# Performance work log

Hardware: AMD Instinct MI355X
Metric: run time of the kernel (lower is better)

## Reference

```python
import jax, jax.numpy as jnp
import numpy as np

EPS = 1e-5  # torch LayerNorm default
N_BLOCKS = 8
N_NODES = 4096
BATCH = 4096


def setup_inputs() -> dict:
    key = jax.random.key(0)
    ks = jax.random.split(key, 4)
    scale = 1.0 / np.sqrt(N_NODES)  # keep activations sane through 8 GEMMs
    x = jax.random.normal(ks[0], (BATCH, N_NODES), dtype=jnp.float32)
    W = jax.random.normal(ks[1], (N_BLOCKS, N_NODES, N_NODES), dtype=jnp.float32) * scale
    b = jax.random.normal(ks[2], (N_BLOCKS, N_NODES), dtype=jnp.float32) * 0.01
    slope = jax.random.uniform(ks[3], (N_BLOCKS, N_NODES), dtype=jnp.float32)
    ln_g = jnp.ones((N_BLOCKS, N_NODES), dtype=jnp.float32)
    ln_b = jnp.zeros((N_BLOCKS, N_NODES), dtype=jnp.float32)
    return {"x": x, "ln_g": ln_g, "ln_b": ln_b, "W": W, "b": b, "slope": slope}


def _block(x, g, bt, Wi, bi, si):
    # LayerNorm over last dim (biased variance, eps inside sqrt) -> Linear -> per-feature LeakyReLU
    mu = jnp.mean(x, axis=-1, keepdims=True)
    var = jnp.mean(jnp.square(x - mu), axis=-1, keepdims=True)
    ln = (x - mu) * jax.lax.rsqrt(var + EPS) * g + bt
    y = jnp.einsum('bn,mn->bm', ln, Wi) + bi  # torch Linear: x @ W.T + b
    return jnp.where(y < 0, y * si, y)


def reference(x, ln_g, ln_b, W, b, slope):
    for i in range(N_BLOCKS):
        x = _block(x, ln_g[i], ln_b[i], W[i], b[i], slope[i])
    return x
```

## Files before the change

### kernel.cpp

```cpp
#include <hip/hip_runtime.h>
#include <hip/hip_bf16.h>

#define NNODES 4096
#define NBATCH 4096
#define NBLK 8
#define LN_EPS 1e-5f

typedef __attribute__((ext_vector_type(8))) short short8;
typedef __attribute__((ext_vector_type(4))) float f32x4;
typedef __attribute__((ext_vector_type(4))) unsigned short u16x4;
typedef unsigned short u16;

__device__ __forceinline__ u16 bf16_rn(float f) {
  unsigned int u = __builtin_bit_cast(unsigned int, f);
  u += 0x7fffu + ((u >> 16) & 1u);
  return (u16)(u >> 16);
}

__device__ __forceinline__ float bf16_to_f(u16 h) {
  unsigned int u = ((unsigned int)h) << 16;
  return __builtin_bit_cast(float, u);
}

__device__ __forceinline__ void load_lds16(const void* g, void* l) {
  __builtin_amdgcn_global_load_lds((const __attribute__((address_space(1))) void*)g,
                                   (__attribute__((address_space(3))) void*)l,
                                   16, 0, 0);
}

__device__ __forceinline__ void stage_sub(const u16* g, u16* l) {
  load_lds16(g, l);
  load_lds16(g + (size_t)128 * NNODES, l + 4096);
}

__global__ __launch_bounds__(256) void convw_kernel(const float* __restrict__ W,
                                                    u16* __restrict__ Wb) {
  int idx = blockIdx.x * 256 + threadIdx.x;
  float4 v = ((const float4*)W)[idx];
  u16x4 o;
  o[0] = bf16_rn(v.x); o[1] = bf16_rn(v.y); o[2] = bf16_rn(v.z); o[3] = bf16_rn(v.w);
  ((u16x4*)Wb)[idx] = o;
}

__global__ __launch_bounds__(256) void ln_f32_kernel(const float* __restrict__ x,
                                                     const float* __restrict__ g,
                                                     const float* __restrict__ bt,
                                                     u16* __restrict__ out) {
  int row = blockIdx.x;
  int t = threadIdx.x;
  const float4* xr = (const float4*)(x + (size_t)row * NNODES);
  float4 v[4];
  float s = 0.f, ss = 0.f;
#pragma unroll
  for (int q = 0; q < 4; ++q) {
    v[q] = xr[q * 256 + t];
    s  += v[q].x + v[q].y + v[q].z + v[q].w;
    ss += v[q].x * v[q].x + v[q].y * v[q].y + v[q].z * v[q].z + v[q].w * v[q].w;
  }
#pragma unroll
  for (int off = 32; off >= 1; off >>= 1) {
    s  += __shfl_xor(s, off, 64);
    ss += __shfl_xor(ss, off, 64);
  }
  __shared__ float sh[8];
  int wid = t >> 6, lane = t & 63;
  if (lane == 0) { sh[wid] = s; sh[wid + 4] = ss; }
  __syncthreads();
  s  = sh[0] + sh[1] + sh[2] + sh[3];
  ss = sh[4] + sh[5] + sh[6] + sh[7];
  float mu  = s * (1.f / NNODES);
  float var = ss * (1.f / NNODES) - mu * mu;
  float rs  = rsqrtf(var + LN_EPS);
  u16x4* o = (u16x4*)(out + (size_t)row * NNODES);
  const float4* gv = (const float4*)g;
  const float4* bv = (const float4*)bt;
#pragma unroll
  for (int q = 0; q < 4; ++q) {
    int i = q * 256 + t;
    float4 gg = gv[i], bb = bv[i];
    u16x4 ov;
    ov[0] = bf16_rn((v[q].x - mu) * rs * gg.x + bb.x);
    ov[1] = bf16_rn((v[q].y - mu) * rs * gg.y + bb.y);
    ov[2] = bf16_rn((v[q].z - mu) * rs * gg.z + bb.z);
    ov[3] = bf16_rn((v[q].w - mu) * rs * gg.w + bb.w);
    o[i] = ov;
  }
}

__global__ __launch_bounds__(256) void ln_bf16_kernel(const u16* __restrict__ x,
                                                      const float* __restrict__ g,
                                                      const float* __restrict__ bt,
                                                      u16* __restrict__ out) {
  int row = blockIdx.x;
  int t = threadIdx.x;
  const u16* xr = x + (size_t)row * NNODES;
  float f[2][8];
  float s = 0.f, ss = 0.f;
#pragma unroll
  for (int q = 0; q < 2; ++q) {
    short8 v = *(const short8*)(xr + q * 2048 + t * 8);
#pragma unroll
    for (int j = 0; j < 8; ++j) {
      float fv = bf16_to_f((u16)v[j]);
      f[q][j] = fv;
      s += fv; ss += fv * fv;
    }
  }
#pragma unroll
  for (int off = 32; off >= 1; off >>= 1) {
    s  += __shfl_xor(s, off, 64);
    ss += __shfl_xor(ss, off, 64);
  }
  __shared__ float sh[8];
  int wid = t >> 6, lane = t & 63;
  if (lane == 0) { sh[wid] = s; sh[wid + 4] = ss; }
  __syncthreads();
  s  = sh[0] + sh[1] + sh[2] + sh[3];
  ss = sh[4] + sh[5] + sh[6] + sh[7];
  float mu  = s * (1.f / NNODES);
  float var = ss * (1.f / NNODES) - mu * mu;
  float rs  = rsqrtf(var + LN_EPS);
  const float4* gv = (const float4*)g;
  const float4* bv = (const float4*)bt;
#pragma unroll
  for (int q = 0; q < 2; ++q) {
    int base = q * 2048 + t * 8;
    float4 g0 = gv[base / 4], g1 = gv[base / 4 + 1];
    float4 b0 = bv[base / 4], b1 = bv[base / 4 + 1];
    short8 sv;
    sv[0] = (short)bf16_rn((f[q][0] - mu) * rs * g0.x + b0.x);
    sv[1] = (short)bf16_rn((f[q][1] - mu) * rs * g0.y + b0.y);
    sv[2] = (short)bf16_rn((f[q][2] - mu) * rs * g0.z + b0.z);
    sv[3] = (short)bf16_rn((f[q][3] - mu) * rs * g0.w + b0.w);
    sv[4] = (short)bf16_rn((f[q][4] - mu) * rs * g1.x + b1.x);
    sv[5] = (short)bf16_rn((f[q][5] - mu) * rs * g1.y + b1.y);
    sv[6] = (short)bf16_rn((f[q][6] - mu) * rs * g1.z + b1.z);
    sv[7] = (short)bf16_rn((f[q][7] - mu) * rs * g1.w + b1.w);
    *(short8*)(out + (size_t)row * NNODES + base) = sv;
  }
}

template <bool OUTF32>
__global__ __launch_bounds__(512, 2) void gemm256_kernel(const u16* __restrict__ A,
                                                         const u16* __restrict__ B,
                                                         const float* __restrict__ bias,
                                                         const float* __restrict__ slope,
                                                         void* __restrict__ Cv) {
  constexpr int Kdim = NNODES;
  constexpr int NSUB = Kdim / 32;
  __shared__ u16 Alds[4][8192];
  __shared__ u16 Blds[4][8192];

  const int tid  = threadIdx.x;
  const int lane = tid & 63;
  const int wid  = tid >> 6;
  const int wr   = wid >> 2;
  const int wc   = wid & 3;

  int bid = blockIdx.x;
  int swz = (bid & 7) * 32 + (bid >> 3);
  const int brow = (swz >> 4) * 256;
  const int bcol = (swz & 15) * 256;

  const int srow = tid >> 2;
  const int scsw = (tid & 3) ^ ((srow >> 1) & 3);
  const u16* Ag = A + (size_t)(brow + srow) * Kdim + scsw * 8;
  const u16* Bg = B + (size_t)(bcol + srow) * Kdim + scsw * 8;

  const int r16 = lane & 15, kq = lane >> 4;
  const int ck  = kq ^ ((r16 >> 1) & 3);
  const int aoff = (wr * 128 + r16) * 32 + ck * 8;
  const int boff = (wc * 64 + r16) * 32 + ck * 8;

  f32x4 acc[8][4] = {};

#pragma unroll
  for (int s = 0; s < 3; ++s) {
    stage_sub(Ag + s * 32, &Alds[s][0] + tid * 8);
    stage_sub(Bg + s * 32, &Blds[s][0] + tid * 8);
  }
  asm volatile("s_waitcnt vmcnt(8)" ::: "memory");
  __builtin_amdgcn_s_barrier();

  for (int s = 0; s < NSUB; ++s) {
    const int sl = s & 3;
    const u16* abase = &Alds[sl][0] + aoff;
    const u16* bbase = &Blds[sl][0] + boff;
    short8 afr[4], bfr[4];

#pragma unroll
    for (int n = 0; n < 4; ++n) bfr[n] = *(const short8*)(bbase + n * 512);
#pragma unroll
    for (int m = 0; m < 4; ++m) afr[m] = *(const short8*)(abase + m * 512);
    if (s + 3 < NSUB) stage_sub(Ag + (s + 3) * 32, &Alds[(s + 3) & 3][0] + tid * 8);
    asm volatile("s_waitcnt lgkmcnt(0)" ::: "memory");
    __builtin_amdgcn_sched_barrier(0);
    __builtin_amdgcn_s_setprio(1);
#pragma unroll
    for (int m = 0; m < 4; ++m)
#pragma unroll
      for (int n = 0; n < 4; ++n)
        acc[m][n] = __builtin_amdgcn_mfma_f32_16x16x32_bf16(afr[m], bfr[n], acc[m][n], 0, 0, 0);
    __builtin_amdgcn_s_setprio(0);

#pragma unroll
    for (int m = 0; m < 4; ++m) afr[m] = *(const short8*)(abase + (m + 4) * 512);
    if (s + 3 < NSUB) stage_sub(Bg + (s + 3) * 32, &Blds[(s + 3) & 3][0] + tid * 8);
    if (s <= NSUB - 4)      asm volatile("s_waitcnt vmcnt(8)" ::: "memory");
    else if (s == NSUB - 3) asm volatile("s_waitcnt vmcnt(4)" ::: "memory");
    else if (s == NSUB - 2) asm volatile("s_waitcnt vmcnt(0)" ::: "memory");
    asm volatile("s_waitcnt lgkmcnt(0)" ::: "memory");
    __builtin_amdgcn_sched_barrier(0);
    __builtin_amdgcn_s_setprio(1);
#pragma unroll
    for (int m = 0; m < 4; ++m)
#pragma unroll
      for (int n = 0; n < 4; ++n)
        acc[m + 4][n] = __builtin_amdgcn_mfma_f32_16x16x32_bf16(afr[m], bfr[n], acc[m + 4][n], 0, 0, 0);
    __builtin_amdgcn_s_setprio(0);
    __builtin_amdgcn_s_barrier();
  }

  const int crow0 = brow + wr * 128 + (lane >> 4) * 4;
  const int ccol0 = bcol + wc * 64 + r16;
#pragma unroll
  for (int n = 0; n < 4; ++n) {
    int col = ccol0 + n * 16;
    float bv = bias[col], sv = slope[col];
#pragma unroll
    for (int m = 0; m < 8; ++m) {
      int row0 = crow0 + m * 16;
#pragma unroll
      for (int r = 0; r < 4; ++r) {
        float vv = acc[m][n][r] + bv;
        vv = vv < 0.f ? vv * sv : vv;
        if constexpr (OUTF32) {
          ((float*)Cv)[(size_t)(row0 + r) * NNODES + col] = vv;
        } else {
          ((u16*)Cv)[(size_t)(row0 + r) * NNODES + col] = bf16_rn(vv);
        }
      }
    }
  }
}

extern "C" void kernel_launch(void* const* d_in, const int* in_sizes, int n_in,
                              void* d_out, int out_size, void* d_ws, size_t ws_size,
                              hipStream_t stream) {
  const float* x     = (const float*)d_in[0];
  const float* ln_g  = (const float*)d_in[1];
  const float* ln_b  = (const float*)d_in[2];
  const float* W     = (const float*)d_in[3];
  const float* b     = (const float*)d_in[4];
  const float* slope = (const float*)d_in[5];
  float* out = (float*)d_out;

  char* ws = (char*)d_ws;
  u16* Wbuf  = (u16*)ws;
  u16* lnbuf = (u16*)(ws + (size_t)32 * 1024 * 1024);
  u16* ybuf  = (u16*)(ws + (size_t)64 * 1024 * 1024);

  const size_t WN = (size_t)NNODES * NNODES;

  for (int i = 0; i < NBLK; ++i) {
    convw_kernel<<<dim3(WN / 4 / 256), dim3(256), 0, stream>>>(W + WN * i, Wbuf);
    if (i == 0)
      ln_f32_kernel<<<dim3(NBATCH), dim3(256), 0, stream>>>(x, ln_g, ln_b, lnbuf);
    else
      ln_bf16_kernel<<<dim3(NBATCH), dim3(256), 0, stream>>>(ybuf, ln_g + (size_t)i * NNODES,
                                                             ln_b + (size_t)i * NNODES, lnbuf);
    if (i == NBLK - 1)
      gemm256_kernel<true><<<dim3(256), dim3(512), 0, stream>>>(lnbuf, Wbuf,
                                                                b + (size_t)i * NNODES,
                                                                slope + (size_t)i * NNODES, (void*)out);
    else
      gemm256_kernel<false><<<dim3(256), dim3(512), 0, stream>>>(lnbuf, Wbuf,
                                                                 b + (size_t)i * NNODES,
                                                                 slope + (size_t)i * NNODES, (void*)ybuf);
  }
}
```

Baseline: 1.229 ms.

## Fuse weight conversion with LayerNorm and restructure GEMM LDS read schedule

Merges the per-block fp32→bf16 weight conversion and the LayerNorm into one launch, with block-index ranges choosing the role. This cuts the launch count and lets both memory-bound phases run at the same time. The GEMM main loop now issues all A fragment LDS reads and both global→LDS stages up front. It then waits on lgkmcnt(4) so the first MFMA half can start while the second A half is still loading. The trade-off is more live registers for the extra fragment array.

```diff
diff --git a/kernel.cpp b/kernel.cpp
--- a/kernel.cpp
+++ b/kernel.cpp
@@ -33,36 +33,53 @@
   load_lds16(g + (size_t)128 * NNODES, l + 4096);
 }
 
-__global__ __launch_bounds__(256) void convw_kernel(const float* __restrict__ W,
-                                                    u16* __restrict__ Wb) {
-  int idx = blockIdx.x * 256 + threadIdx.x;
-  float4 v = ((const float4*)W)[idx];
-  u16x4 o;
-  o[0] = bf16_rn(v.x); o[1] = bf16_rn(v.y); o[2] = bf16_rn(v.z); o[3] = bf16_rn(v.w);
-  ((u16x4*)Wb)[idx] = o;
-}
-
-__global__ __launch_bounds__(256) void ln_f32_kernel(const float* __restrict__ x,
-                                                     const float* __restrict__ g,
-                                                     const float* __restrict__ bt,
-                                                     u16* __restrict__ out) {
-  int row = blockIdx.x;
+template <bool LNF32>
+__global__ __launch_bounds__(256) void prep_kernel(const float* __restrict__ W,
+                                                   u16* __restrict__ Wb,
+                                                   const void* __restrict__ xin,
+                                                   const float* __restrict__ g,
+                                                   const float* __restrict__ bt,
+                                                   u16* __restrict__ lnout) {
+  __shared__ float sh[8];
   int t = threadIdx.x;
-  const float4* xr = (const float4*)(x + (size_t)row * NNODES);
-  float4 v[4];
+  if (blockIdx.x < 16384) {
+    int idx = blockIdx.x * 256 + t;
+    float4 v = ((const float4*)W)[idx];
+    u16x4 o;
+    o[0] = bf16_rn(v.x); o[1] = bf16_rn(v.y); o[2] = bf16_rn(v.z); o[3] = bf16_rn(v.w);
+    ((u16x4*)Wb)[idx] = o;
+    return;
+  }
+  int row = blockIdx.x - 16384;
+  float f[16];
   float s = 0.f, ss = 0.f;
-#pragma unroll
-  for (int q = 0; q < 4; ++q) {
-    v[q] = xr[q * 256 + t];
-    s  += v[q].x + v[q].y + v[q].z + v[q].w;
-    ss += v[q].x * v[q].x + v[q].y * v[q].y + v[q].z * v[q].z + v[q].w * v[q].w;
+  if constexpr (LNF32) {
+    const float4* xr = (const float4*)((const float*)xin + (size_t)row * NNODES);
+#pragma unroll
+    for (int q = 0; q < 4; ++q) {
+      float4 v = xr[q * 256 + t];
+      f[q * 4 + 0] = v.x; f[q * 4 + 1] = v.y; f[q * 4 + 2] = v.z; f[q * 4 + 3] = v.w;
+      s  += v.x + v.y + v.z + v.w;
+      ss += v.x * v.x + v.y * v.y + v.z * v.z + v.w * v.w;
+    }
+  } else {
+    const u16* xr = (const u16*)xin + (size_t)row * NNODES;
+#pragma unroll
+    for (int q = 0; q < 2; ++q) {
+      short8 v = *(const short8*)(xr + q * 2048 + t * 8);
+#pragma unroll
+      for (int j = 0; j < 8; ++j) {
+        float fv = bf16_to_f((u16)v[j]);
+        f[q * 8 + j] = fv;
+        s += fv; ss += fv * fv;
+      }
+    }
   }
 #pragma unroll
   for (int off = 32; off >= 1; off >>= 1) {
     s  += __shfl_xor(s, off, 64);
     ss += __shfl_xor(ss, off, 64);
   }
-  __shared__ float sh[8];
   int wid = t >> 6, lane = t & 63;
   if (lane == 0) { sh[wid] = s; sh[wid + 4] = ss; }
   __syncthreads();
@@ -71,72 +88,40 @@
   float mu  = s * (1.f / NNODES);
   float var = ss * (1.f / NNODES) - mu * mu;
   float rs  = rsqrtf(var + LN_EPS);
-  u16x4* o = (u16x4*)(out + (size_t)row * NNODES);
-  const float4* gv = (const float4*)g;
-  const float4* bv = (const float4*)bt;
-#pragma unroll
-  for (int q = 0; q < 4; ++q) {
-    int i = q * 256 + t;
-    float4 gg = gv[i], bb = bv[i];
-    u16x4 ov;
-    ov[0] = bf16_rn((v[q].x - mu) * rs * gg.x + bb.x);
-    ov[1] = bf16_rn((v[q].y - mu) * rs * gg.y + bb.y);
-    ov[2] = bf16_rn((v[q].z - mu) * rs * gg.z + bb.z);
-    ov[3] = bf16_rn((v[q].w - mu) * rs * gg.w + bb.w);
-    o[i] = ov;
-  }
-}
-
-__global__ __launch_bounds__(256) void ln_bf16_kernel(const u16* __restrict__ x,
-                                                      const float* __restrict__ g,
-                                                      const float* __restrict__ bt,
-                                                      u16* __restrict__ out) {
-  int row = blockIdx.x;
-  int t = threadIdx.x;
-  const u16* xr = x + (size_t)row * NNODES;
-  float f[2][8];
-  float s = 0.f, ss = 0.f;
-#pragma unroll
-  for (int q = 0; q < 2; ++q) {
-    short8 v = *(const short8*)(xr + q * 2048 + t * 8);
-#pragma unroll
-    for (int j = 0; j < 8; ++j) {
-      float fv = bf16_to_f((u16)v[j]);
-      f[q][j] = fv;
-      s += fv; ss += fv * fv;
-    }
-  }
-#pragma unroll
-  for (int off = 32; off >= 1; off >>= 1) {
-    s  += __shfl_xor(s, off, 64);
-    ss += __shfl_xor(ss, off, 64);
-  }
-  __shared__ float sh[8];
-  int wid = t >> 6, lane = t & 63;
-  if (lane == 0) { sh[wid] = s; sh[wid + 4] = ss; }
-  __syncthreads();
-  s  = sh[0] + sh[1] + sh[2] + sh[3];
-  ss = sh[4] + sh[5] + sh[6] + sh[7];
-  float mu  = s * (1.f / NNODES);
-  float var = ss * (1.f / NNODES) - mu * mu;
-  float rs  = rsqrtf(var + LN_EPS);
-  const float4* gv = (const float4*)g;
-  const float4* bv = (const float4*)bt;
-#pragma unroll
-  for (int q = 0; q < 2; ++q) {
-    int base = q * 2048 + t * 8;
-    float4 g0 = gv[base / 4], g1 = gv[base / 4 + 1];
-    float4 b0 = bv[base / 4], b1 = bv[base / 4 + 1];
-    short8 sv;
-    sv[0] = (short)bf16_rn((f[q][0] - mu) * rs * g0.x + b0.x);
-    sv[1] = (short)bf16_rn((f[q][1] - mu) * rs * g0.y + b0.y);
-    sv[2] = (short)bf16_rn((f[q][2] - mu) * rs * g0.z + b0.z);
-    sv[3] = (short)bf16_rn((f[q][3] - mu) * rs * g0.w + b0.w);
-    sv[4] = (short)bf16_rn((f[q][4] - mu) * rs * g1.x + b1.x);
-    sv[5] = (short)bf16_rn((f[q][5] - mu) * rs * g1.y + b1.y);
-    sv[6] = (short)bf16_rn((f[q][6] - mu) * rs * g1.z + b1.z);
-    sv[7] = (short)bf16_rn((f[q][7] - mu) * rs * g1.w + b1.w);
-    *(short8*)(out + (size_t)row * NNODES + base) = sv;
+  const float* gp = g;
+  const float* bp = bt;
+  if constexpr (LNF32) {
+    u16x4* o = (u16x4*)(lnout + (size_t)row * NNODES);
+    const float4* gv = (const float4*)gp;
+    const float4* bv = (const float4*)bp;
+#pragma unroll
+    for (int q = 0; q < 4; ++q) {
+      int i = q * 256 + t;
+      float4 gg = gv[i], bb = bv[i];
+      u16x4 ov;
+      ov[0] = bf16_rn((f[q * 4 + 0] - mu) * rs * gg.x + bb.x);
+      ov[1] = bf16_rn((f[q * 4 + 1] - mu) * rs * gg.y + bb.y);
+      ov[2] = bf16_rn((f[q * 4 + 2] - mu) * rs * gg.z + bb.z);
+      ov[3] = bf16_rn((f[q * 4 + 3] - mu) * rs * gg.w + bb.w);
+      o[i] = ov;
+    }
+  } else {
+#pragma unroll
+    for (int q = 0; q < 2; ++q) {
+      int base = q * 2048 + t * 8;
+      float4 g0 = ((const float4*)gp)[base / 4], g1 = ((const float4*)gp)[base / 4 + 1];
+      float4 b0 = ((const float4*)bp)[base / 4], b1 = ((const float4*)bp)[base / 4 + 1];
+      short8 sv;
+      sv[0] = (short)bf16_rn((f[q * 8 + 0] - mu) * rs * g0.x + b0.x);
+      sv[1] = (short)bf16_rn((f[q * 8 + 1] - mu) * rs * g0.y + b0.y);
+      sv[2] = (short)bf16_rn((f[q * 8 + 2] - mu) * rs * g0.z + b0.z);
+      sv[3] = (short)bf16_rn((f[q * 8 + 3] - mu) * rs * g0.w + b0.w);
+      sv[4] = (short)bf16_rn((f[q * 8 + 4] - mu) * rs * g1.x + b1.x);
+      sv[5] = (short)bf16_rn((f[q * 8 + 5] - mu) * rs * g1.y + b1.y);
+      sv[6] = (short)bf16_rn((f[q * 8 + 6] - mu) * rs * g1.z + b1.z);
+      sv[7] = (short)bf16_rn((f[q * 8 + 7] - mu) * rs * g1.w + b1.w);
+      *(short8*)(lnout + (size_t)row * NNODES + base) = sv;
+    }
   }
 }
 
@@ -186,13 +171,34 @@
     const int sl = s & 3;
     const u16* abase = &Alds[sl][0] + aoff;
     const u16* bbase = &Blds[sl][0] + boff;
-    short8 afr[4], bfr[4];
+    short8 a03[4], a47[4], bfr[4];
 
 #pragma unroll
     for (int n = 0; n < 4; ++n) bfr[n] = *(const short8*)(bbase + n * 512);
 #pragma unroll
-    for (int m = 0; m < 4; ++m) afr[m] = *(const short8*)(abase + m * 512);
-    if (s + 3 < NSUB) stage_sub(Ag + (s + 3) * 32, &Alds[(s + 3) & 3][0] + tid * 8);
+    for (int m = 0; m < 4; ++m) a03[m] = *(const short8*)(abase + m * 512);
+    __builtin_amdgcn_sched_barrier(0);
+#pragma unroll
+    for (int m = 0; m < 4; ++m) a47[m] = *(const short8*)(abase + (m + 4) * 512);
+
+    if (s + 3 < NSUB) {
+      stage_sub(Ag + (s + 3) * 32, &Alds[(s + 3) & 3][0] + tid * 8);
+      stage_sub(Bg + (s + 3) * 32, &Blds[(s + 3) & 3][0] + tid * 8);
+    }
+    if (s <= NSUB - 4)      asm volatile("s_waitcnt vmcnt(8)" ::: "memory");
+    else if (s == NSUB - 3) asm volatile("s_waitcnt vmcnt(4)" ::: "memory");
+    else if (s == NSUB - 2) asm volatile("s_waitcnt vmcnt(0)" ::: "memory");
+
+    asm volatile("s_waitcnt lgkmcnt(4)" ::: "memory");
+    __builtin_amdgcn_sched_barrier(0);
+    __builtin_amdgcn_s_setprio(1);
+#pragma unroll
+    for (int m = 0; m < 4; ++m)
+#pragma unroll
+      for (int n = 0; n < 4; ++n)
+        acc[m][n] = __builtin_amdgcn_mfma_f32_16x16x32_bf16(a03[m], bfr[n], acc[m][n], 0, 0, 0);
+    __builtin_amdgcn_s_setprio(0);
+
     asm volatile("s_waitcnt lgkmcnt(0)" ::: "memory");
     __builtin_amdgcn_sched_barrier(0);
     __builtin_amdgcn_s_setprio(1);
@@ -200,23 +206,7 @@
     for (int m = 0; m < 4; ++m)
 #pragma unroll
       for (int n = 0; n < 4; ++n)
-        acc[m][n] = __builtin_amdgcn_mfma_f32_16x16x32_bf16(afr[m], bfr[n], acc[m][n], 0, 0, 0);
-    __builtin_amdgcn_s_setprio(0);
-
-#pragma unroll
-    for (int m = 0; m < 4; ++m) afr[m] = *(const short8*)(abase + (m + 4) * 512);
-    if (s + 3 < NSUB) stage_sub(Bg + (s + 3) * 32, &Blds[(s + 3) & 3][0] + tid * 8);
-    if (s <= NSUB - 4)      asm volatile("s_waitcnt vmcnt(8)" ::: "memory");
-    else if (s == NSUB - 3) asm volatile("s_waitcnt vmcnt(4)" ::: "memory");
-    else if (s == NSUB - 2) asm volatile("s_waitcnt vmcnt(0)" ::: "memory");
-    asm volatile("s_waitcnt lgkmcnt(0)" ::: "memory");
-    __builtin_amdgcn_sched_barrier(0);
-    __builtin_amdgcn_s_setprio(1);
-#pragma unroll
-    for (int m = 0; m < 4; ++m)
-#pragma unroll
-      for (int n = 0; n < 4; ++n)
-        acc[m + 4][n] = __builtin_amdgcn_mfma_f32_16x16x32_bf16(afr[m], bfr[n], acc[m + 4][n], 0, 0, 0);
+        acc[m + 4][n] = __builtin_amdgcn_mfma_f32_16x16x32_bf16(a47[m], bfr[n], acc[m + 4][n], 0, 0, 0);
     __builtin_amdgcn_s_setprio(0);
     __builtin_amdgcn_s_barrier();
   }
@@ -261,14 +251,16 @@
   u16* ybuf  = (u16*)(ws + (size_t)64 * 1024 * 1024);
 
   const size_t WN = (size_t)NNODES * NNODES;
+  const dim3 pgrid(16384 + NBATCH);
 
   for (int i = 0; i < NBLK; ++i) {
-    convw_kernel<<<dim3(WN / 4 / 256), dim3(256), 0, stream>>>(W + WN * i, Wbuf);
     if (i == 0)
-      ln_f32_kernel<<<dim3(NBATCH), dim3(256), 0, stream>>>(x, ln_g, ln_b, lnbuf);
+      prep_kernel<true><<<pgrid, dim3(256), 0, stream>>>(W, Wbuf, (const void*)x,
+                                                         ln_g, ln_b, lnbuf);
     else
-      ln_bf16_kernel<<<dim3(NBATCH), dim3(256), 0, stream>>>(ybuf, ln_g + (size_t)i * NNODES,
-                                                             ln_b + (size_t)i * NNODES, lnbuf);
+      prep_kernel<false><<<pgrid, dim3(256), 0, stream>>>(W + WN * i, Wbuf, (const void*)ybuf,
+                                                          ln_g + (size_t)i * NNODES,
+                                                          ln_b + (size_t)i * NNODES, lnbuf);
     if (i == NBLK - 1)
       gemm256_kernel<true><<<dim3(256), dim3(512), 0, stream>>>(lnbuf, Wbuf,
                                                                 b + (size_t)i * NNODES,
```

After: 1.182 ms. 3.8% less time.

## Fuse fp32-to-bf16 weight conversion into GEMM B-tile loading

Applied to the files above, without the earlier changes.

Removes the separate weight conversion kernel per block. The GEMM now loads fp32 weights into registers, converts them to bf16 and writes them into swizzled LDS, while A tiles still go straight to LDS via global_load_lds. The main loop is rebuilt into K=64 double-buffered tiles with quarter-tile phases that interleave loads, LDS writes and MFMAs. This saves a full read and write pass over each 64MB weight matrix, but the GEMM now reads twice as many bytes for B and pays extra VALU and register cost for the conversion.

```diff
diff --git a/kernel.cpp b/kernel.cpp
--- a/kernel.cpp
+++ b/kernel.cpp
@@ -28,18 +28,17 @@
                                    16, 0, 0);
 }
 
-__device__ __forceinline__ void stage_sub(const u16* g, u16* l) {
-  load_lds16(g, l);
-  load_lds16(g + (size_t)128 * NNODES, l + 4096);
-}
-
-__global__ __launch_bounds__(256) void convw_kernel(const float* __restrict__ W,
-                                                    u16* __restrict__ Wb) {
-  int idx = blockIdx.x * 256 + threadIdx.x;
-  float4 v = ((const float4*)W)[idx];
-  u16x4 o;
-  o[0] = bf16_rn(v.x); o[1] = bf16_rn(v.y); o[2] = bf16_rn(v.z); o[3] = bf16_rn(v.w);
-  ((u16x4*)Wb)[idx] = o;
+__device__ __forceinline__ void gload4(f32x4& d, const float* p) {
+  asm volatile("global_load_dwordx4 %0, %1, off" : "=&v"(d) : "v"(p) : "memory");
+}
+
+__device__ __forceinline__ short8 cvt8(f32x4 a, f32x4 b) {
+  short8 r;
+  r[0] = (short)bf16_rn(a[0]); r[1] = (short)bf16_rn(a[1]);
+  r[2] = (short)bf16_rn(a[2]); r[3] = (short)bf16_rn(a[3]);
+  r[4] = (short)bf16_rn(b[0]); r[5] = (short)bf16_rn(b[1]);
+  r[6] = (short)bf16_rn(b[2]); r[7] = (short)bf16_rn(b[3]);
+  return r;
 }
 
 __global__ __launch_bounds__(256) void ln_f32_kernel(const float* __restrict__ x,
@@ -140,16 +139,77 @@
   }
 }
 
+
+#define VMC(N) asm volatile("s_waitcnt vmcnt(" #N ")" ::: "memory")
+#define NOP ((void)0)
+
+#define STAGE_A(T, H)                                                          \
+  { load_lds16(Asrc0 + (size_t)((H) * 128) * Kdim + (T) * 64,                  \
+               ldsA + ((T) & 1) * 16384 + (H) * 8192 + tid * 8);               \
+    load_lds16(Asrc0 + (size_t)((H) * 128 + 64) * Kdim + (T) * 64,             \
+               ldsA + ((T) & 1) * 16384 + (H) * 8192 + 4096 + tid * 8); }
+
+#define LOADB(R, T, H)                                                         \
+  { const float* p_ = Wp + (size_t)((H) * 128 + bwrow) * Kdim + (T) * 64 + bwc4 * 16; \
+    gload4(R[0], p_); gload4(R[1], p_ + 4);                                    \
+    gload4(R[2], p_ + 8); gload4(R[3], p_ + 12); }
+
+#define WRITEB(R, T, H)                                                        \
+  { u16* d_ = ldsB + ((T) & 1) * 16384 + (H) * 8192 + bwrow * 64;              \
+    *(short8*)(d_ + bwg0 * 8) = cvt8(R[0], R[1]);                              \
+    *(short8*)(d_ + bwg1 * 8) = cvt8(R[2], R[3]);                              \
+    asm volatile("s_waitcnt lgkmcnt(0)" ::: "memory"); }
+
+#define PH(KT, MH, NH, EXTRA, VM_STMT, WR_STMT)                                \
+  {                                                                            \
+    EXTRA;                                                                     \
+    VM_STMT;                                                                   \
+    __builtin_amdgcn_sched_barrier(0);                                         \
+    WR_STMT;                                                                   \
+    __builtin_amdgcn_sched_barrier(0);                                         \
+    const u16* Ab = ldsA + ((KT) & 1) * 16384 + aBase + (MH) * 4096;           \
+    const u16* Bb = ldsB + ((KT) & 1) * 16384 + bBase + (NH) * 2048;           \
+    if ((NH) == 0) {                                                           \
+      _Pragma("unroll") for (int mi = 0; mi < 4; ++mi) {                       \
+        afr[mi][0] = *(const short8*)(Ab + mi * 1024 + gk0);                   \
+        afr[mi][1] = *(const short8*)(Ab + mi * 1024 + gk1);                   \
+      }                                                                        \
+    }                                                                          \
+    if ((MH) == 0) {                                                           \
+      _Pragma("unroll") for (int ni = 0; ni < 2; ++ni) {                       \
+        bfr[NH][ni][0] = *(const short8*)(Bb + ni * 1024 + gk0);               \
+        bfr[NH][ni][1] = *(const short8*)(Bb + ni * 1024 + gk1);               \
+      }                                                                        \
+    }                                                                          \
+    if ((NH) == 0 && (MH) == 0)                                                \
+      asm volatile("s_waitcnt lgkmcnt(8)" ::: "memory");                       \
+    __builtin_amdgcn_s_barrier();                                              \
+    asm volatile("s_waitcnt lgkmcnt(0)" ::: "memory");                         \
+    __builtin_amdgcn_sched_barrier(0);                                         \
+    __builtin_amdgcn_s_setprio(1);                                             \
+    _Pragma("unroll") for (int mi = 0; mi < 4; ++mi)                           \
+      _Pragma("unroll") for (int ni = 0; ni < 2; ++ni) {                       \
+        acc[(MH) * 4 + mi][(NH) * 2 + ni] =                                    \
+          __builtin_amdgcn_mfma_f32_16x16x32_bf16(afr[mi][0], bfr[NH][ni][0],  \
+            acc[(MH) * 4 + mi][(NH) * 2 + ni], 0, 0, 0);                       \
+        acc[(MH) * 4 + mi][(NH) * 2 + ni] =                                    \
+          __builtin_amdgcn_mfma_f32_16x16x32_bf16(afr[mi][1], bfr[NH][ni][1],  \
+            acc[(MH) * 4 + mi][(NH) * 2 + ni], 0, 0, 0);                       \
+      }                                                                        \
+    __builtin_amdgcn_s_setprio(0);                                             \
+    __builtin_amdgcn_s_barrier();                                              \
+  }
+
 template <bool OUTF32>
 __global__ __launch_bounds__(512, 2) void gemm256_kernel(const u16* __restrict__ A,
-                                                         const u16* __restrict__ B,
+                                                         const float* __restrict__ W,
                                                          const float* __restrict__ bias,
                                                          const float* __restrict__ slope,
                                                          void* __restrict__ Cv) {
   constexpr int Kdim = NNODES;
-  constexpr int NSUB = Kdim / 32;
-  __shared__ u16 Alds[4][8192];
-  __shared__ u16 Blds[4][8192];
+  __shared__ u16 lds[65536];
+  u16* ldsA = lds;
+  u16* ldsB = lds + 32768;
 
   const int tid  = threadIdx.x;
   const int lane = tid & 63;
@@ -162,64 +222,58 @@
   const int brow = (swz >> 4) * 256;
   const int bcol = (swz & 15) * 256;
 
-  const int srow = tid >> 2;
-  const int scsw = (tid & 3) ^ ((srow >> 1) & 3);
-  const u16* Ag = A + (size_t)(brow + srow) * Kdim + scsw * 8;
-  const u16* Bg = B + (size_t)(bcol + srow) * Kdim + scsw * 8;
+  const int srow = tid >> 3;
+  const int sg   = ((tid & 7) ^ (srow & 7)) * 8;
+  const u16* Asrc0 = A + (size_t)(brow + srow) * Kdim + sg;
+
+  const int bwrow = tid >> 2;
+  const int bwc4  = tid & 3;
+  const int bwg0  = (2 * bwc4)     ^ (bwrow & 7);
+  const int bwg1  = (2 * bwc4 + 1) ^ (bwrow & 7);
+  const float* Wp = W + (size_t)bcol * Kdim;
 
   const int r16 = lane & 15, kq = lane >> 4;
-  const int ck  = kq ^ ((r16 >> 1) & 3);
-  const int aoff = (wr * 128 + r16) * 32 + ck * 8;
-  const int boff = (wc * 64 + r16) * 32 + ck * 8;
+  const int g0  = kq ^ (r16 & 7);
+  const int gk0 = g0 * 8, gk1 = (g0 ^ 4) * 8;
+  const int aBase = wr * 8192 + r16 * 64;
+  const int bBase = (wc >> 1) * 8192 + ((wc & 1) * 64 + r16) * 64;
 
   f32x4 acc[8][4] = {};
-
-#pragma unroll
-  for (int s = 0; s < 3; ++s) {
-    stage_sub(Ag + s * 32, &Alds[s][0] + tid * 8);
-    stage_sub(Bg + s * 32, &Blds[s][0] + tid * 8);
-  }
-  asm volatile("s_waitcnt vmcnt(8)" ::: "memory");
+  short8 afr[4][2], bfr[2][2][2];
+  f32x4 blo[4], bhi[4];
+
+  LOADB(blo, 0, 0)
+  LOADB(bhi, 0, 1)
+  STAGE_A(0, 0)
+  STAGE_A(0, 1)
+  VMC(4);
+  __builtin_amdgcn_sched_barrier(0);
+  WRITEB(blo, 0, 0)
+  WRITEB(bhi, 0, 1)
+  LOADB(blo, 1, 0)
+  LOADB(bhi, 1, 1)
+  VMC(8);
   __builtin_amdgcn_s_barrier();
 
-  for (int s = 0; s < NSUB; ++s) {
-    const int sl = s & 3;
-    const u16* abase = &Alds[sl][0] + aoff;
-    const u16* bbase = &Blds[sl][0] + boff;
-    short8 afr[4], bfr[4];
-
-#pragma unroll
-    for (int n = 0; n < 4; ++n) bfr[n] = *(const short8*)(bbase + n * 512);
-#pragma unroll
-    for (int m = 0; m < 4; ++m) afr[m] = *(const short8*)(abase + m * 512);
-    if (s + 3 < NSUB) stage_sub(Ag + (s + 3) * 32, &Alds[(s + 3) & 3][0] + tid * 8);
-    asm volatile("s_waitcnt lgkmcnt(0)" ::: "memory");
-    __builtin_amdgcn_sched_barrier(0);
-    __builtin_amdgcn_s_setprio(1);
-#pragma unroll
-    for (int m = 0; m < 4; ++m)
-#pragma unroll
-      for (int n = 0; n < 4; ++n)
-        acc[m][n] = __builtin_amdgcn_mfma_f32_16x16x32_bf16(afr[m], bfr[n], acc[m][n], 0, 0, 0);
-    __builtin_amdgcn_s_setprio(0);
-
-#pragma unroll
-    for (int m = 0; m < 4; ++m) afr[m] = *(const short8*)(abase + (m + 4) * 512);
-    if (s + 3 < NSUB) stage_sub(Bg + (s + 3) * 32, &Blds[(s + 3) & 3][0] + tid * 8);
-    if (s <= NSUB - 4)      asm volatile("s_waitcnt vmcnt(8)" ::: "memory");
-    else if (s == NSUB - 3) asm volatile("s_waitcnt vmcnt(4)" ::: "memory");
-    else if (s == NSUB - 2) asm volatile("s_waitcnt vmcnt(0)" ::: "memory");
-    asm volatile("s_waitcnt lgkmcnt(0)" ::: "memory");
-    __builtin_amdgcn_sched_barrier(0);
-    __builtin_amdgcn_s_setprio(1);
-#pragma unroll
-    for (int m = 0; m < 4; ++m)
-#pragma unroll
-      for (int n = 0; n < 4; ++n)
-        acc[m + 4][n] = __builtin_amdgcn_mfma_f32_16x16x32_bf16(afr[m], bfr[n], acc[m + 4][n], 0, 0, 0);
-    __builtin_amdgcn_s_setprio(0);
-    __builtin_amdgcn_s_barrier();
-  }
+  for (int t = 0; t < 31; ++t) {
+    const int T = 2 * t;
+    PH(T,     0, 0, STAGE_A(T + 1, 0),   VMC(6), WRITEB(blo, T + 1, 0))
+    PH(T,     0, 1, STAGE_A(T + 1, 1),   VMC(4), WRITEB(bhi, T + 1, 1))
+    PH(T,     1, 0, LOADB(blo, T + 2, 0), NOP,    NOP)
+    PH(T,     1, 1, LOADB(bhi, T + 2, 1), VMC(8), NOP)
+    PH(T + 1, 0, 0, STAGE_A(T + 2, 0),   VMC(6), WRITEB(blo, T + 2, 0))
+    PH(T + 1, 0, 1, STAGE_A(T + 2, 1),   VMC(4), WRITEB(bhi, T + 2, 1))
+    PH(T + 1, 1, 0, LOADB(blo, T + 3, 0), NOP,    NOP)
+    PH(T + 1, 1, 1, LOADB(bhi, T + 3, 1), VMC(8), NOP)
+  }
+  PH(62, 0, 0, STAGE_A(63, 0), VMC(6), WRITEB(blo, 63, 0))
+  PH(62, 0, 1, STAGE_A(63, 1), VMC(4), WRITEB(bhi, 63, 1))
+  PH(62, 1, 0, NOP, NOP, NOP)
+  PH(62, 1, 1, NOP, VMC(0), NOP)
+  PH(63, 0, 0, NOP, NOP, NOP)
+  PH(63, 0, 1, NOP, NOP, NOP)
+  PH(63, 1, 0, NOP, NOP, NOP)
+  PH(63, 1, 1, NOP, NOP, NOP)
 
   const int crow0 = brow + wr * 128 + (lane >> 4) * 4;
   const int ccol0 = bcol + wc * 64 + r16;
@@ -256,25 +310,23 @@
   float* out = (float*)d_out;
 
   char* ws = (char*)d_ws;
-  u16* Wbuf  = (u16*)ws;
-  u16* lnbuf = (u16*)(ws + (size_t)32 * 1024 * 1024);
-  u16* ybuf  = (u16*)(ws + (size_t)64 * 1024 * 1024);
+  u16* lnbuf = (u16*)ws;
+  u16* ybuf  = (u16*)(ws + (size_t)32 * 1024 * 1024);
 
   const size_t WN = (size_t)NNODES * NNODES;
 
   for (int i = 0; i < NBLK; ++i) {
-    convw_kernel<<<dim3(WN / 4 / 256), dim3(256), 0, stream>>>(W + WN * i, Wbuf);
     if (i == 0)
       ln_f32_kernel<<<dim3(NBATCH), dim3(256), 0, stream>>>(x, ln_g, ln_b, lnbuf);
     else
       ln_bf16_kernel<<<dim3(NBATCH), dim3(256), 0, stream>>>(ybuf, ln_g + (size_t)i * NNODES,
                                                              ln_b + (size_t)i * NNODES, lnbuf);
     if (i == NBLK - 1)
-      gemm256_kernel<true><<<dim3(256), dim3(512), 0, stream>>>(lnbuf, Wbuf,
+      gemm256_kernel<true><<<dim3(256), dim3(512), 0, stream>>>(lnbuf, W + WN * i,
                                                                 b + (size_t)i * NNODES,
                                                                 slope + (size_t)i * NNODES, (void*)out);
     else
-      gemm256_kernel<false><<<dim3(256), dim3(512), 0, stream>>>(lnbuf, Wbuf,
+      gemm256_kernel<false><<<dim3(256), dim3(512), 0, stream>>>(lnbuf, W + WN * i,
                                                                  b + (size_t)i * NNODES,
                                                                  slope + (size_t)i * NNODES, (void*)ybuf);
   }
```

After: 1.576 ms. 28.2% more time.
